# Kernel tuning notes

Measured on AMD Instinct MI355X. Metric: run time of the kernel, lower is better.

## Reference

```python
import jax, jax.numpy as jnp
import numpy as np

N, M, DIST, HEADS, D, C, DFFN = 16384, 16, 2, 8, 256, 64, 512
DH = D // HEADS
GRID = 128
BLOCK = 2048  # mirrors torch batch_size loop in find_neighboring_voxels_optimized
EPS = 1e-5


def _neighbors(coords_f, src, m, dist):
    """Blockwise Manhattan-distance topk neighbor gather.
    coords_f: (N,3) float voxel coords; src: (N,D) features.
    Returns (N, m, D) neighbor features, zero-filled where fewer than m in range."""
    n = coords_f.shape[0]
    qblocks = coords_f.reshape(-1, BLOCK, 3)

    def one_block(cb):
        # (BLOCK, N) Manhattan distances
        d = jnp.abs(cb[:, None, :] - coords_f[None, :, :]).sum(-1)
        d = jnp.where(d <= dist, d, jnp.inf)
        vals, idx = jax.lax.top_k(-d, m)          # nearest m (self first: dist 0)
        valid = (vals > -jnp.inf)[..., None]
        return jnp.where(valid, src[idx], jnp.zeros((), src.dtype))

    return jax.lax.map(one_block, qblocks).reshape(n, m, src.shape[-1])


def _layernorm(x, g, b):
    mu = x.mean(-1, keepdims=True)
    var = ((x - mu) ** 2).mean(-1, keepdims=True)
    return (x - mu) * jax.lax.rsqrt(var + EPS) * g + b


def setup_inputs() -> dict:
    key = jax.random.key(0)
    ks = jax.random.split(key, 32)
    p = lambda i, shape, s: jax.random.normal(ks[i], shape, dtype=jnp.float32) * s
    z = lambda shape: jnp.zeros(shape, dtype=jnp.float32)
    o = lambda shape: jnp.ones(shape, dtype=jnp.float32)
    return {
        "coords": jax.random.randint(ks[0], (N, 3), 0, GRID, dtype=jnp.int32),
        "features": jax.random.normal(ks[1], (N, C), dtype=jnp.float32),
        "pe_w1": p(2, (3, D // 2), 0.5), "pe_b1": z((D // 2,)),
        "pe_w2": p(3, (D // 2, D), 0.08), "pe_b2": z((D,)),
        "proj_w": p(4, (C, D), 0.12), "proj_b": z((D,)),
        "wq": p(5, (D, D), 0.06), "bq": z((D,)),
        "wk": p(6, (D, D), 0.06), "bk": z((D,)),
        "wv": p(7, (D, D), 0.06), "bv": z((D,)),
        "wo": p(8, (D, D), 0.06), "bo": z((D,)),
        "ffn_w1": p(9, (D, DFFN), 0.06), "ffn_b1": z((DFFN,)),
        "ffn_w2": p(10, (DFFN, D), 0.04), "ffn_b2": z((D,)),
        "ln_g": o((D,)), "ln_b": z((D,)),
        "fus_w1": p(11, (D, C), 0.06), "fus_b1": z((C,)),
        "fus_w2": p(12, (2 * C, C), 0.09), "fus_b2": z((C,)),
        "bn_g": o((C,)), "bn_b": z((C,)),
    }


def reference(coords, features, pe_w1, pe_b1, pe_w2, pe_b2, proj_w, proj_b,
              wq, bq, wk, bk, wv, bv, wo, bo,
              ffn_w1, ffn_b1, ffn_w2, ffn_b2, ln_g, ln_b,
              fus_w1, fus_b1, fus_w2, fus_b2, bn_g, bn_b):
    coords_f = coords.astype(jnp.float32)
    # dynamic learnable positional encoding on normalized coords
    xn = coords_f / (GRID - 1)
    pe = jax.nn.relu(xn @ pe_w1 + pe_b1) @ pe_w2 + pe_b2
    src = features @ proj_w + proj_b + pe                       # (N, D)

    nf = _neighbors(coords_f, src, M, DIST)                     # (N, M, D)
    query = nf[:, 0, :]                                         # (N, D) self-feature

    # multihead attention: query len 1, key len M, batch N
    q = (query @ wq + bq).reshape(N, HEADS, DH)
    k = (nf @ wk + bk).reshape(N, M, HEADS, DH)
    v = (nf @ wv + bv).reshape(N, M, HEADS, DH)
    scores = jnp.einsum('nhd,nmhd->nhm', q, k) / jnp.sqrt(jnp.float32(DH))
    attn = jax.nn.softmax(scores, axis=-1)
    ao = jnp.einsum('nhm,nmhd->nhd', attn, v).reshape(N, D) @ wo + bo  # (N, D)

    # FFN with residual + LayerNorm (dropout=0 / eval)
    h = jax.nn.relu(ao @ ffn_w1 + ffn_b1) @ ffn_w2 + ffn_b2
    y = _layernorm(ao + h, ln_g, ln_b)                          # (N, D)

    # EnhancedFusion: project, concat, linear, BatchNorm1d (batch stats), ReLU
    t = y @ fus_w1 + fus_b1                                     # (N, C)
    f = jnp.concatenate([features, t], axis=1) @ fus_w2 + fus_b2
    mu = f.mean(0)
    var = ((f - mu) ** 2).mean(0)
    f = (f - mu) * jax.lax.rsqrt(var + EPS) * bn_g + bn_b
    return jax.nn.relu(f)                                       # (N, C)
```

## Files before the change

kernel.cpp:

```cpp
#include <hip/hip_runtime.h>
#include <stdint.h>

typedef unsigned short u16;
typedef unsigned int   u32;
typedef __attribute__((ext_vector_type(8))) short short8;
typedef __attribute__((ext_vector_type(4))) float f32x4;

static constexpr int kN = 16384;
static constexpr float kEPS = 1e-5f;

__device__ __forceinline__ u16 f2bf(float x) {
  u32 u = __float_as_uint(x);
  u32 r = (u + 0x7fffu + ((u >> 16) & 1u)) >> 16;
  return (u16)r;
}
__device__ __forceinline__ float bf2f(u16 x) {
  return __uint_as_float(((u32)x) << 16);
}
__device__ __forceinline__ void ldbf8(const u16* p, float* o) {
  uint4 v = *(const uint4*)p;
  o[0] = __uint_as_float(v.x << 16);  o[1] = __uint_as_float(v.x & 0xffff0000u);
  o[2] = __uint_as_float(v.y << 16);  o[3] = __uint_as_float(v.y & 0xffff0000u);
  o[4] = __uint_as_float(v.z << 16);  o[5] = __uint_as_float(v.z & 0xffff0000u);
  o[6] = __uint_as_float(v.w << 16);  o[7] = __uint_as_float(v.w & 0xffff0000u);
}


__global__ __launch_bounds__(256) void k_hist(const int* __restrict__ coords,
                                              u32* __restrict__ cnt) {
  int n = blockIdx.x * 256 + threadIdx.x;
  int c = coords[n * 3] * 128 + coords[n * 3 + 1];
  atomicAdd(&cnt[c], 1u);
}

__global__ __launch_bounds__(256) void k_scan(const u32* __restrict__ cnt,
                                              u32* __restrict__ startb) {
  __shared__ u32 tots[256];
  int t = threadIdx.x;
  int base = t * 64;
  u32 s = 0;
  for (int i = 0; i < 64; i++) s += cnt[base + i];
  tots[t] = s;
  __syncthreads();
  if (t == 0) {
    u32 run = 0;
    for (int i = 0; i < 256; i++) { u32 v = tots[i]; tots[i] = run; run += v; }
  }
  __syncthreads();
  u32 run = tots[t];
  for (int i = 0; i < 64; i++) { startb[base + i] = run; run += cnt[base + i]; }
}

__global__ __launch_bounds__(256) void k_scatter(const int* __restrict__ coords,
                                                 const u32* __restrict__ startb,
                                                 u32* __restrict__ cursor,
                                                 u32* __restrict__ pts) {
  int n = blockIdx.x * 256 + threadIdx.x;
  int x = coords[n * 3], y = coords[n * 3 + 1], z = coords[n * 3 + 2];
  int c = x * 128 + y;
  u32 slot = atomicAdd(&cursor[c], 1u);
  pts[startb[c] + slot] = ((u32)z << 14) | (u32)n;
}

__global__ __launch_bounds__(256) void k_select(const int* __restrict__ coords,
                                                const u32* __restrict__ startb,
                                                const u32* __restrict__ cnt,
                                                const u32* __restrict__ pts,
                                                int* __restrict__ idxo) {
  int n = blockIdx.x * 256 + threadIdx.x;
  int x = coords[n * 3], y = coords[n * 3 + 1], z = coords[n * 3 + 2];
  u32 best[16];
#pragma unroll
  for (int j = 0; j < 16; j++) best[j] = 0xFFFFFFFFu;
  const int dxs[13] = {0, -1, 1, 0, 0, -2, 2, 0, 0, -1, -1, 1, 1};
  const int dys[13] = {0, 0, 0, -1, 1, 0, 0, -2, 2, -1, 1, -1, 1};
  const int dbs[13] = {0, 1, 1, 1, 1, 2, 2, 2, 2, 2, 2, 2, 2};
#pragma unroll
  for (int t = 0; t < 13; t++) {
    int xx = x + dxs[t], yy = y + dys[t];
    if (xx < 0 || xx > 127 || yy < 0 || yy > 127) continue;
    int c = xx * 128 + yy;
    u32 s0 = startb[c], e0 = s0 + cnt[c];
    for (u32 i = s0; i < e0; ++i) {
      u32 p = pts[i];
      int zq = (int)(p >> 14);
      int id = (int)(p & 16383u);
      int az = z - zq; az = az < 0 ? -az : az;
      int dd = dbs[t] + az;
      u32 key = (dd <= 2) ? (((u32)dd << 14) | (u32)id) : 0xFFFFFFFFu;
#pragma unroll
      for (int j = 0; j < 16; j++) {
        u32 lo = min(best[j], key);
        u32 hi = max(best[j], key);
        best[j] = lo; key = hi;
      }
    }
  }
#pragma unroll
  for (int j = 0; j < 16; j++)
    idxo[n * 16 + j] = (best[j] == 0xFFFFFFFFu) ? -1 : (int)(best[j] & 16383u);
}

struct WSet {
  const float* s[8]; u16* d[8];
  int K[8]; int N[8]; int dstride[8]; int coff[8];
};

__global__ __launch_bounds__(256) void k_setup(WSet ws,
                                               u32* __restrict__ zero_area,
                                               const float* __restrict__ proj_b,
                                               const float* __restrict__ pe_b2,
                                               float* __restrict__ pbc,
                                               const float* __restrict__ uw1,
                                               const float* __restrict__ ub1,
                                               const float* __restrict__ uw2,
                                               const float* __restrict__ ub2,
                                               u16* __restrict__ W2f,
                                               float* __restrict__ bbf) {
  int w = blockIdx.y;
  if (w == 8) {
    zero_area[blockIdx.x * 256 + threadIdx.x] = 0u;
    return;
  }
  if (w == 9) {
    int bx = blockIdx.x;
    if (bx == 0) {
      pbc[threadIdx.x] = proj_b[threadIdx.x] + pe_b2[threadIdx.x];
    } else if (bx < 65) {
      int n = bx - 1;
      int k = threadIdx.x;
      float s = 0.f;
      for (int j = 0; j < 64; j++) s += uw1[k * 64 + j] * uw2[(64 + j) * 64 + n];
      W2f[n * 320 + k] = f2bf(s);
      if (k < 64) W2f[n * 320 + 256 + k] = f2bf(uw2[k * 64 + n]);
      if (k == 0) {
        float b = ub2[n];
        for (int j = 0; j < 64; j++) b += ub1[j] * uw2[(64 + j) * 64 + n];
        bbf[n] = b;
      }
    }
    return;
  }
  const float* S = ws.s[w]; u16* D = ws.d[w];
  int K = ws.K[w], N = ws.N[w], ds = ws.dstride[w], co = ws.coff[w];
  int ntx = N >> 5, tiles = ntx * (K >> 5);
  int t = blockIdx.x;
  if (t >= tiles) return;
  int n0 = (t % ntx) * 32, k0 = (t / ntx) * 32;
  __shared__ float st[32][33];
  int tr = threadIdx.x >> 3, tc4 = (threadIdx.x & 7) * 4;
  float4 v = *(const float4*)(S + (size_t)(k0 + tr) * N + n0 + tc4);
  st[tc4 + 0][tr] = v.x; st[tc4 + 1][tr] = v.y;
  st[tc4 + 2][tr] = v.z; st[tc4 + 3][tr] = v.w;
  __syncthreads();
  u16 o4[4];
  o4[0] = f2bf(st[tr][tc4 + 0]); o4[1] = f2bf(st[tr][tc4 + 1]);
  o4[2] = f2bf(st[tr][tc4 + 2]); o4[3] = f2bf(st[tr][tc4 + 3]);
  *(uint2*)(D + (size_t)(n0 + tr) * ds + co + k0 + tc4) = *(uint2*)o4;
}

__global__ __launch_bounds__(256) void k_prep(const int* __restrict__ coords,
                                              const float* __restrict__ feats,
                                              const float* __restrict__ pw1,
                                              const float* __restrict__ pb1,
                                              u16* __restrict__ A1,
                                              u16* __restrict__ A2) {
  int r0 = blockIdx.x * 32;
#pragma unroll
  for (int s = 0; s < 3; s++) {
    int j = threadIdx.x + s * 256;
    int row = j / 24, seg = j % 24;
    int n = r0 + row;
    u16 o[8];
    if (seg < 8) {
      const float* fp = feats + (size_t)n * 64 + seg * 8;
      float4 a = *(const float4*)fp;
      float4 b = *(const float4*)(fp + 4);
      o[0] = f2bf(a.x); o[1] = f2bf(a.y); o[2] = f2bf(a.z); o[3] = f2bf(a.w);
      o[4] = f2bf(b.x); o[5] = f2bf(b.y); o[6] = f2bf(b.z); o[7] = f2bf(b.w);
      *(uint4*)(A2 + (size_t)n * 320 + 256 + seg * 8) = *(uint4*)o;
    } else {
      int jj0 = (seg - 8) * 8;
      float x0 = (float)coords[n * 3 + 0] * (1.f / 127.f);
      float x1 = (float)coords[n * 3 + 1] * (1.f / 127.f);
      float x2 = (float)coords[n * 3 + 2] * (1.f / 127.f);
#pragma unroll
      for (int u = 0; u < 8; u++) {
        int jj = jj0 + u;
        float hv = pb1[jj] + x0 * pw1[jj] + x1 * pw1[128 + jj] + x2 * pw1[256 + jj];
        o[u] = f2bf(fmaxf(hv, 0.f));
      }
    }
    *(uint4*)(A1 + (size_t)n * 192 + seg * 8) = *(uint4*)o;
  }
}

template <int BM, int BN, int ACT, int OUTBF, int ADD>
__global__ __launch_bounds__(256) void k_mfma_gemm(
    const u16* __restrict__ A, const u16* __restrict__ WT,
    const float* __restrict__ bias,
    void* __restrict__ Cout,
    const u16* __restrict__ Addp,
    int M, int K, int N) {
  constexpr int GA = BM / 64;
  constexpr int GT = (BM + BN) / 64;
  constexpr int AI = BM / 32;
  constexpr int BI = BN / 32;
  __shared__ __align__(16) u16 As[BM * 32];
  __shared__ __align__(16) u16 Bs[BN * 32];
  const int tid = threadIdx.x;
  const int wave = tid >> 6, lane = tid & 63;
  const int bm = blockIdx.y * BM, bn = blockIdx.x * BN;
  const int wr = (wave >> 1) * (BM / 2), wc = (wave & 1) * (BN / 2);

  f32x4 acc[AI][BI];
#pragma unroll
  for (int i = 0; i < AI; i++)
#pragma unroll
    for (int j = 0; j < BI; j++)
#pragma unroll
      for (int r = 0; r < 4; r++) acc[i][j][r] = 0.f;

  for (int k0 = 0; k0 < K; k0 += 32) {
#pragma unroll
    for (int i = 0; i < GT; i++) {
      int g = i * 256 + wave * 64 + lane;
      if (i < GA) {
        int row = g >> 2, ko = (g & 3) * 8;
        __builtin_amdgcn_global_load_lds(
            (const __attribute__((address_space(1))) void*)(A + (size_t)(bm + row) * K + k0 + ko),
            (__attribute__((address_space(3))) void*)(As + (size_t)g * 8), 16, 0, 0);
      } else {
        int g2 = g - GA * 256;
        int row = g2 >> 2, ko = (g2 & 3) * 8;
        __builtin_amdgcn_global_load_lds(
            (const __attribute__((address_space(1))) void*)(WT + (size_t)(bn + row) * K + k0 + ko),
            (__attribute__((address_space(3))) void*)(Bs + (size_t)g2 * 8), 16, 0, 0);
      }
    }
    __syncthreads();
    short8 af[AI], bg[BI];
#pragma unroll
    for (int i = 0; i < AI; i++)
      af[i] = *(const short8*)&As[(wr + i * 16 + (lane & 15)) * 32 + (lane >> 4) * 8];
#pragma unroll
    for (int j = 0; j < BI; j++)
      bg[j] = *(const short8*)&Bs[(wc + j * 16 + (lane & 15)) * 32 + (lane >> 4) * 8];
#pragma unroll
    for (int i = 0; i < AI; i++)
#pragma unroll
      for (int j = 0; j < BI; j++)
        acc[i][j] = __builtin_amdgcn_mfma_f32_16x16x32_bf16(af[i], bg[j], acc[i][j], 0, 0, 0);
    __syncthreads();
  }

#pragma unroll
  for (int j = 0; j < BI; j++) {
    int cc = bn + wc + j * 16 + (lane & 15);
    float bval = bias ? bias[cc] : 0.f;
#pragma unroll
    for (int i = 0; i < AI; i++) {
      int rbase = bm + wr + i * 16 + (lane >> 4) * 4;
#pragma unroll
      for (int r = 0; r < 4; r++) {
        float v = acc[i][j][r] + bval;
        size_t o = (size_t)(rbase + r) * N + cc;
        if (ADD) v += bf2f(Addp[o]);
        if (ACT) v = fmaxf(v, 0.f);
        if (OUTBF) ((u16*)Cout)[o] = f2bf(v);
        else       ((float*)Cout)[o] = v;
      }
    }
  }
}

__global__ __launch_bounds__(256) void k_attn(const u16* __restrict__ QKV,
                                              const u32* __restrict__ pts,
                                              const int* __restrict__ idx,
                                              const float* __restrict__ bq,
                                              const float* __restrict__ bk,
                                              const float* __restrict__ bv,
                                              u16* __restrict__ outp) {
  int gid = blockIdx.x * 256 + threadIdx.x;
  int n = (int)(pts[gid >> 3] & 16383u), h = gid & 7;
  const int* ip = idx + n * 16;
  const int hb = h * 32;
  float q[32];
  {
    int i0 = ip[0];
    const u16* qp = QKV + (size_t)i0 * 768 + hb;
#pragma unroll
    for (int j = 0; j < 32; j += 8) ldbf8(qp + j, &q[j]);
#pragma unroll
    for (int j = 0; j < 32; j++) q[j] += bq[hb + j];
  }
  float qbk = 0.f;
#pragma unroll
  for (int j = 0; j < 32; j++) qbk += q[j] * bk[hb + j];
  float s[16]; int ii[16];
#pragma unroll
  for (int m = 0; m < 16; m++) {
    int i = ip[m]; ii[m] = i;
    float d = qbk;
    if (i >= 0) {
      const u16* kp = QKV + (size_t)i * 768 + 256 + hb;
      float kv[32];
#pragma unroll
      for (int j = 0; j < 32; j += 8) ldbf8(kp + j, &kv[j]);
#pragma unroll
      for (int j = 0; j < 32; j++) d += q[j] * kv[j];
    }
    s[m] = d * 0.17677669529663689f;
  }
  float mx = s[0];
#pragma unroll
  for (int m = 1; m < 16; m++) mx = fmaxf(mx, s[m]);
  float sum = 0.f;
#pragma unroll
  for (int m = 0; m < 16; m++) { s[m] = __expf(s[m] - mx); sum += s[m]; }
  float inv = 1.f / sum;
  float o[32];
#pragma unroll
  for (int j = 0; j < 32; j++) o[j] = 0.f;
#pragma unroll
  for (int m = 0; m < 16; m++) {
    if (ii[m] >= 0) {
      const u16* vp = QKV + (size_t)ii[m] * 768 + 512 + hb;
      float vv[32];
#pragma unroll
      for (int j = 0; j < 32; j += 8) ldbf8(vp + j, &vv[j]);
#pragma unroll
      for (int j = 0; j < 32; j++) o[j] += s[m] * vv[j];
    }
  }
  u16* op = outp + (size_t)n * 256 + hb;
#pragma unroll
  for (int j = 0; j < 32; j += 8) {
    u16 tmp[8];
#pragma unroll
    for (int jj = 0; jj < 8; jj++) tmp[jj] = f2bf(o[j + jj] * inv + bv[hb + j + jj]);
    *(uint4*)(op + j) = *(uint4*)tmp;
  }
}

__global__ __launch_bounds__(256) void k_ln(const u16* __restrict__ xx,
                                            const float* __restrict__ g,
                                            const float* __restrict__ b,
                                            u16* __restrict__ A2) {
  int row = blockIdx.x * 4 + (threadIdx.x >> 6);
  int lane = threadIdx.x & 63;
  uint2 raw = *(const uint2*)(xx + (size_t)row * 256 + lane * 4);
  float x0 = __uint_as_float(raw.x << 16), x1 = __uint_as_float(raw.x & 0xffff0000u);
  float x2 = __uint_as_float(raw.y << 16), x3 = __uint_as_float(raw.y & 0xffff0000u);
  float sm = x0 + x1 + x2 + x3;
#pragma unroll
  for (int off = 1; off < 64; off <<= 1) sm += __shfl_xor(sm, off);
  float mu = sm * (1.f / 256.f);
  float d0 = x0 - mu, d1 = x1 - mu, d2 = x2 - mu, d3 = x3 - mu;
  float sq = d0 * d0 + d1 * d1 + d2 * d2 + d3 * d3;
#pragma unroll
  for (int off = 1; off < 64; off <<= 1) sq += __shfl_xor(sq, off);
  float rstd = rsqrtf(sq * (1.f / 256.f) + kEPS);
  float4 gv = *(const float4*)(g + lane * 4);
  float4 bv4 = *(const float4*)(b + lane * 4);
  u16 o[4];
  o[0] = f2bf(d0 * rstd * gv.x + bv4.x); o[1] = f2bf(d1 * rstd * gv.y + bv4.y);
  o[2] = f2bf(d2 * rstd * gv.z + bv4.z); o[3] = f2bf(d3 * rstd * gv.w + bv4.w);
  *(uint2*)(A2 + (size_t)row * 320 + lane * 4) = *(uint2*)o;
}

__global__ __launch_bounds__(256) void k_stats(const float* __restrict__ f,
                                               float* __restrict__ pS, float* __restrict__ pQ) {
  int col = threadIdx.x & 63, rc = threadIdx.x >> 6;
  int r0 = blockIdx.x * 128 + rc * 32;
  float s = 0.f, q = 0.f;
  for (int r = 0; r < 32; r++) {
    float v = f[(size_t)(r0 + r) * 64 + col];
    s += v; q += v * v;
  }
  __shared__ float ls[4][64], lq[4][64];
  ls[rc][col] = s; lq[rc][col] = q;
  __syncthreads();
  if (rc == 0) {
    s = ls[0][col] + ls[1][col] + ls[2][col] + ls[3][col];
    q = lq[0][col] + lq[1][col] + lq[2][col] + lq[3][col];
    pS[blockIdx.x * 64 + col] = s;
    pQ[blockIdx.x * 64 + col] = q;
  }
}

__global__ __launch_bounds__(64) void k_bnfin(const float* __restrict__ pS,
                                              const float* __restrict__ pQ,
                                              const float* __restrict__ g,
                                              const float* __restrict__ b,
                                              float* __restrict__ coef,
                                              float* __restrict__ shift) {
  int c = threadIdx.x;
  float s = 0.f, q = 0.f;
  for (int i = 0; i < 128; i++) { s += pS[i * 64 + c]; q += pQ[i * 64 + c]; }
  float mu = s * (1.f / 16384.f);
  float var = q * (1.f / 16384.f) - mu * mu;
  float cf = rsqrtf(var + kEPS) * g[c];
  coef[c] = cf;
  shift[c] = b[c] - mu * cf;
}

__global__ __launch_bounds__(256) void k_bnapply(const float* __restrict__ f,
                                                 const float* __restrict__ coef,
                                                 const float* __restrict__ shift,
                                                 float* __restrict__ out) {
  int gid = blockIdx.x * 256 + threadIdx.x;
  int e = gid * 4, col = e & 63;
  float4 v = *(const float4*)(f + e);
  float4 cf = *(const float4*)(coef + col);
  float4 sh = *(const float4*)(shift + col);
  float4 o;
  o.x = fmaxf(v.x * cf.x + sh.x, 0.f);
  o.y = fmaxf(v.y * cf.y + sh.y, 0.f);
  o.z = fmaxf(v.z * cf.z + sh.z, 0.f);
  o.w = fmaxf(v.w * cf.w + sh.w, 0.f);
  *(float4*)(out + e) = o;
}

extern "C" void kernel_launch(void* const* d_in, const int* in_sizes, int n_in,
                              void* d_out, int out_size, void* d_ws, size_t ws_size,
                              hipStream_t stream) {
  (void)in_sizes; (void)n_in; (void)out_size; (void)ws_size;
  const int*   coords = (const int*)d_in[0];
  const float* feats  = (const float*)d_in[1];
  const float* pe_w1  = (const float*)d_in[2];
  const float* pe_b1  = (const float*)d_in[3];
  const float* pe_w2  = (const float*)d_in[4];
  const float* pe_b2  = (const float*)d_in[5];
  const float* proj_w = (const float*)d_in[6];
  const float* proj_b = (const float*)d_in[7];
  const float* wq  = (const float*)d_in[8];
  const float* bq  = (const float*)d_in[9];
  const float* wk  = (const float*)d_in[10];
  const float* bk  = (const float*)d_in[11];
  const float* wv  = (const float*)d_in[12];
  const float* bv  = (const float*)d_in[13];
  const float* wo  = (const float*)d_in[14];
  const float* bo  = (const float*)d_in[15];
  const float* fw1 = (const float*)d_in[16];
  const float* fb1 = (const float*)d_in[17];
  const float* fw2 = (const float*)d_in[18];
  const float* fb2 = (const float*)d_in[19];
  const float* lng = (const float*)d_in[20];
  const float* lnb = (const float*)d_in[21];
  const float* uw1 = (const float*)d_in[22];
  const float* ub1 = (const float*)d_in[23];
  const float* uw2 = (const float*)d_in[24];
  const float* ub2 = (const float*)d_in[25];
  const float* bng = (const float*)d_in[26];
  const float* bnb = (const float*)d_in[27];
  float* out = (float*)d_out;

  char* Wc = (char*)d_ws;
  const size_t MB = 1u << 20;
  u16*   A1    = (u16*)(Wc + 0 * MB);
  u16*   srcb  = (u16*)(Wc + 6 * MB);
  u16*   QKVb  = (u16*)(Wc + 14 * MB);
  u16*   aoInB = (u16*)(Wc + 38 * MB);
  u16*   aoB   = (u16*)(Wc + 46 * MB);
  u16*   h1B   = (u16*)(Wc + 54 * MB);
  u16*   xBb   = (u16*)(Wc + 70 * MB);
  u16*   A2    = (u16*)(Wc + 78 * MB);
  float* fB    = (float*)(Wc + 0 * MB);

  u16* qkvT  = (u16*)(Wc + 96 * MB);
  u16* woT   = qkvT + 196608;
  u16* fw1T  = woT + 65536;
  u16* fw2T  = fw1T + 131072;
  u16* W1T   = fw2T + 131072;
  u16* W2f   = W1T + 49152;
  float* pbc = (float*)(W2f + 20480);
  float* bbf = pbc + 256;

  u32* cnt    = (u32*)(Wc + 98 * MB);
  u32* cursor = cnt + 16384;
  u32* startb = cnt + 32768;
  u32* pts    = cnt + 49152;
  int* idxb   = (int*)(cnt + 65536);
  float* pS    = (float*)(cnt + 65536 + 262144);
  float* pQ    = pS + 8192;
  float* coefb = pQ + 8192;
  float* shb   = coefb + 64;

  WSet ws;
  ws.s[0] = wq;     ws.d[0] = qkvT;          ws.K[0] = 256; ws.N[0] = 256; ws.dstride[0] = 256; ws.coff[0] = 0;
  ws.s[1] = wk;     ws.d[1] = qkvT + 65536;  ws.K[1] = 256; ws.N[1] = 256; ws.dstride[1] = 256; ws.coff[1] = 0;
  ws.s[2] = wv;     ws.d[2] = qkvT + 131072; ws.K[2] = 256; ws.N[2] = 256; ws.dstride[2] = 256; ws.coff[2] = 0;
  ws.s[3] = wo;     ws.d[3] = woT;           ws.K[3] = 256; ws.N[3] = 256; ws.dstride[3] = 256; ws.coff[3] = 0;
  ws.s[4] = fw1;    ws.d[4] = fw1T;          ws.K[4] = 256; ws.N[4] = 512; ws.dstride[4] = 256; ws.coff[4] = 0;
  ws.s[5] = fw2;    ws.d[5] = fw2T;          ws.K[5] = 512; ws.N[5] = 256; ws.dstride[5] = 512; ws.coff[5] = 0;
  ws.s[6] = proj_w; ws.d[6] = W1T;           ws.K[6] = 64;  ws.N[6] = 256; ws.dstride[6] = 192; ws.coff[6] = 0;
  ws.s[7] = pe_w2;  ws.d[7] = W1T;           ws.K[7] = 128; ws.N[7] = 256; ws.dstride[7] = 192; ws.coff[7] = 64;
  k_setup<<<dim3(128, 10), 256, 0, stream>>>(ws, cnt, proj_b, pe_b2, pbc,
                                             uw1, ub1, uw2, ub2, W2f, bbf);

  k_hist<<<64, 256, 0, stream>>>(coords, cnt);
  k_scan<<<1, 256, 0, stream>>>(cnt, startb);
  k_scatter<<<64, 256, 0, stream>>>(coords, startb, cursor, pts);
  k_select<<<64, 256, 0, stream>>>(coords, startb, cnt, pts, idxb);

  k_prep<<<512, 256, 0, stream>>>(coords, feats, pe_w1, pe_b1, A1, A2);

  k_mfma_gemm<64, 64, 0, 1, 0><<<dim3(4, 256), 256, 0, stream>>>(A1, W1T, pbc, srcb, nullptr, kN, 192, 256);
  k_mfma_gemm<64, 64, 0, 1, 0><<<dim3(12, 256), 256, 0, stream>>>(srcb, qkvT, nullptr, QKVb, nullptr, kN, 256, 768);

  k_attn<<<512, 256, 0, stream>>>(QKVb, pts, idxb, bq, bk, bv, aoInB);

  k_mfma_gemm<64, 64, 0, 1, 0><<<dim3(4, 256), 256, 0, stream>>>(aoInB, woT, bo, aoB, nullptr, kN, 256, 256);
  k_mfma_gemm<64, 64, 1, 1, 0><<<dim3(8, 256), 256, 0, stream>>>(aoB, fw1T, fb1, h1B, nullptr, kN, 256, 512);
  k_mfma_gemm<64, 64, 0, 1, 1><<<dim3(4, 256), 256, 0, stream>>>(h1B, fw2T, fb2, xBb, aoB, kN, 512, 256);

  k_ln<<<4096, 256, 0, stream>>>(xBb, lng, lnb, A2);

  k_mfma_gemm<64, 64, 0, 0, 0><<<dim3(1, 256), 256, 0, stream>>>(A2, W2f, bbf, fB, nullptr, kN, 320, 64);

  k_stats<<<128, 256, 0, stream>>>(fB, pS, pQ);
  k_bnfin<<<1, 64, 0, stream>>>(pS, pQ, bng, bnb, coefb, shb);
  k_bnapply<<<1024, 256, 0, stream>>>(fB, coefb, shb, out);
}
```

Before: 257.6 us.

## Fuse neighbor-grid stages and BN tail into persistent kernels with grid barriers

Merges the histogram, scan, scatter and select kernels into one 64-block kernel that uses software grid barriers built on atomics. The final GEMM, batch-norm statistics, finalize and apply steps become one kernel that keeps its results in registers and uses a last-arriving block to compute the BN coefficients. The prep kernel is folded into the setup launch. This cuts kernel launch count and drops the fp32 intermediate round trip. In exchange it depends on all blocks being co-resident for the spin-wait barriers, and the float atomicAdd reductions make the statistics order nondeterministic.

After: 294.6 us. 1.14x slower.

```diff
diff --git a/kernel.cpp b/kernel.cpp
--- a/kernel.cpp
+++ b/kernel.cpp
@@ -24,81 +24,10 @@
   o[4] = __uint_as_float(v.z << 16);  o[5] = __uint_as_float(v.z & 0xffff0000u);
   o[6] = __uint_as_float(v.w << 16);  o[7] = __uint_as_float(v.w & 0xffff0000u);
 }
-
-
-__global__ __launch_bounds__(256) void k_hist(const int* __restrict__ coords,
-                                              u32* __restrict__ cnt) {
-  int n = blockIdx.x * 256 + threadIdx.x;
-  int c = coords[n * 3] * 128 + coords[n * 3 + 1];
-  atomicAdd(&cnt[c], 1u);
-}
-
-__global__ __launch_bounds__(256) void k_scan(const u32* __restrict__ cnt,
-                                              u32* __restrict__ startb) {
-  __shared__ u32 tots[256];
-  int t = threadIdx.x;
-  int base = t * 64;
-  u32 s = 0;
-  for (int i = 0; i < 64; i++) s += cnt[base + i];
-  tots[t] = s;
-  __syncthreads();
-  if (t == 0) {
-    u32 run = 0;
-    for (int i = 0; i < 256; i++) { u32 v = tots[i]; tots[i] = run; run += v; }
-  }
-  __syncthreads();
-  u32 run = tots[t];
-  for (int i = 0; i < 64; i++) { startb[base + i] = run; run += cnt[base + i]; }
-}
-
-__global__ __launch_bounds__(256) void k_scatter(const int* __restrict__ coords,
-                                                 const u32* __restrict__ startb,
-                                                 u32* __restrict__ cursor,
-                                                 u32* __restrict__ pts) {
-  int n = blockIdx.x * 256 + threadIdx.x;
-  int x = coords[n * 3], y = coords[n * 3 + 1], z = coords[n * 3 + 2];
-  int c = x * 128 + y;
-  u32 slot = atomicAdd(&cursor[c], 1u);
-  pts[startb[c] + slot] = ((u32)z << 14) | (u32)n;
-}
-
-__global__ __launch_bounds__(256) void k_select(const int* __restrict__ coords,
-                                                const u32* __restrict__ startb,
-                                                const u32* __restrict__ cnt,
-                                                const u32* __restrict__ pts,
-                                                int* __restrict__ idxo) {
-  int n = blockIdx.x * 256 + threadIdx.x;
-  int x = coords[n * 3], y = coords[n * 3 + 1], z = coords[n * 3 + 2];
-  u32 best[16];
-#pragma unroll
-  for (int j = 0; j < 16; j++) best[j] = 0xFFFFFFFFu;
-  const int dxs[13] = {0, -1, 1, 0, 0, -2, 2, 0, 0, -1, -1, 1, 1};
-  const int dys[13] = {0, 0, 0, -1, 1, 0, 0, -2, 2, -1, 1, -1, 1};
-  const int dbs[13] = {0, 1, 1, 1, 1, 2, 2, 2, 2, 2, 2, 2, 2};
-#pragma unroll
-  for (int t = 0; t < 13; t++) {
-    int xx = x + dxs[t], yy = y + dys[t];
-    if (xx < 0 || xx > 127 || yy < 0 || yy > 127) continue;
-    int c = xx * 128 + yy;
-    u32 s0 = startb[c], e0 = s0 + cnt[c];
-    for (u32 i = s0; i < e0; ++i) {
-      u32 p = pts[i];
-      int zq = (int)(p >> 14);
-      int id = (int)(p & 16383u);
-      int az = z - zq; az = az < 0 ? -az : az;
-      int dd = dbs[t] + az;
-      u32 key = (dd <= 2) ? (((u32)dd << 14) | (u32)id) : 0xFFFFFFFFu;
-#pragma unroll
-      for (int j = 0; j < 16; j++) {
-        u32 lo = min(best[j], key);
-        u32 hi = max(best[j], key);
-        best[j] = lo; key = hi;
-      }
-    }
-  }
-#pragma unroll
-  for (int j = 0; j < 16; j++)
-    idxo[n * 16 + j] = (best[j] == 0xFFFFFFFFu) ? -1 : (int)(best[j] & 16383u);
+__device__ __forceinline__ void gll16(const u16* g, u16* l) {
+  __builtin_amdgcn_global_load_lds(
+      (const __attribute__((address_space(1))) void*)g,
+      (__attribute__((address_space(3))) void*)l, 16, 0, 0);
 }
 
 struct WSet {
@@ -116,10 +45,17 @@
                                                const float* __restrict__ uw2,
                                                const float* __restrict__ ub2,
                                                u16* __restrict__ W2f,
-                                               float* __restrict__ bbf) {
+                                               float* __restrict__ bbf,
+                                               const int* __restrict__ coords,
+                                               const float* __restrict__ feats,
+                                               const float* __restrict__ pw1,
+                                               const float* __restrict__ pb1,
+                                               u16* __restrict__ A1,
+                                               u16* __restrict__ A2) {
   int w = blockIdx.y;
   if (w == 8) {
-    zero_area[blockIdx.x * 256 + threadIdx.x] = 0u;
+    int idx = blockIdx.x * 256 + threadIdx.x;
+    if (idx < 33088) zero_area[idx] = 0u;
     return;
   }
   if (w == 9) {
@@ -141,6 +77,37 @@
     }
     return;
   }
+  if (w == 10) {
+    int r0 = blockIdx.x * 32;
+#pragma unroll
+    for (int s = 0; s < 3; s++) {
+      int j = threadIdx.x + s * 256;
+      int row = j / 24, seg = j % 24;
+      int n = r0 + row;
+      u16 o[8];
+      if (seg < 8) {
+        const float* fp = feats + (size_t)n * 64 + seg * 8;
+        float4 a = *(const float4*)fp;
+        float4 b = *(const float4*)(fp + 4);
+        o[0] = f2bf(a.x); o[1] = f2bf(a.y); o[2] = f2bf(a.z); o[3] = f2bf(a.w);
+        o[4] = f2bf(b.x); o[5] = f2bf(b.y); o[6] = f2bf(b.z); o[7] = f2bf(b.w);
+        *(uint4*)(A2 + (size_t)n * 320 + 256 + seg * 8) = *(uint4*)o;
+      } else {
+        int jj0 = (seg - 8) * 8;
+        float x0 = (float)coords[n * 3 + 0] * (1.f / 127.f);
+        float x1 = (float)coords[n * 3 + 1] * (1.f / 127.f);
+        float x2 = (float)coords[n * 3 + 2] * (1.f / 127.f);
+#pragma unroll
+        for (int u = 0; u < 8; u++) {
+          int jj = jj0 + u;
+          float hv = pb1[jj] + x0 * pw1[jj] + x1 * pw1[128 + jj] + x2 * pw1[256 + jj];
+          o[u] = f2bf(fmaxf(hv, 0.f));
+        }
+      }
+      *(uint4*)(A1 + (size_t)n * 192 + seg * 8) = *(uint4*)o;
+    }
+    return;
+  }
   const float* S = ws.s[w]; u16* D = ws.d[w];
   int K = ws.K[w], N = ws.N[w], ds = ws.dstride[w], co = ws.coff[w];
   int ntx = N >> 5, tiles = ntx * (K >> 5);
@@ -159,108 +126,136 @@
   *(uint2*)(D + (size_t)(n0 + tr) * ds + co + k0 + tc4) = *(uint2*)o4;
 }
 
-__global__ __launch_bounds__(256) void k_prep(const int* __restrict__ coords,
-                                              const float* __restrict__ feats,
-                                              const float* __restrict__ pw1,
-                                              const float* __restrict__ pb1,
-                                              u16* __restrict__ A1,
-                                              u16* __restrict__ A2) {
-  int r0 = blockIdx.x * 32;
-#pragma unroll
-  for (int s = 0; s < 3; s++) {
-    int j = threadIdx.x + s * 256;
-    int row = j / 24, seg = j % 24;
-    int n = r0 + row;
-    u16 o[8];
-    if (seg < 8) {
-      const float* fp = feats + (size_t)n * 64 + seg * 8;
-      float4 a = *(const float4*)fp;
-      float4 b = *(const float4*)(fp + 4);
-      o[0] = f2bf(a.x); o[1] = f2bf(a.y); o[2] = f2bf(a.z); o[3] = f2bf(a.w);
-      o[4] = f2bf(b.x); o[5] = f2bf(b.y); o[6] = f2bf(b.z); o[7] = f2bf(b.w);
-      *(uint4*)(A2 + (size_t)n * 320 + 256 + seg * 8) = *(uint4*)o;
-    } else {
-      int jj0 = (seg - 8) * 8;
-      float x0 = (float)coords[n * 3 + 0] * (1.f / 127.f);
-      float x1 = (float)coords[n * 3 + 1] * (1.f / 127.f);
-      float x2 = (float)coords[n * 3 + 2] * (1.f / 127.f);
-#pragma unroll
-      for (int u = 0; u < 8; u++) {
-        int jj = jj0 + u;
-        float hv = pb1[jj] + x0 * pw1[jj] + x1 * pw1[128 + jj] + x2 * pw1[256 + jj];
-        o[u] = f2bf(fmaxf(hv, 0.f));
+__device__ __forceinline__ void gbar(u32* bar, u32 target) {
+  __syncthreads();
+  if (threadIdx.x == 0) {
+    __threadfence();
+    __hip_atomic_fetch_add(bar, 1u, __ATOMIC_RELEASE, __HIP_MEMORY_SCOPE_AGENT);
+    while (__hip_atomic_load(bar, __ATOMIC_ACQUIRE, __HIP_MEMORY_SCOPE_AGENT) < target) {}
+    __threadfence();
+  }
+  __syncthreads();
+}
+
+__global__ __launch_bounds__(256) void k_grid(const int* __restrict__ coords,
+                                              u32* __restrict__ cnt,
+                                              u32* __restrict__ cursor,
+                                              u32* __restrict__ startb,
+                                              u32* __restrict__ pts,
+                                              int* __restrict__ idxo,
+                                              u32* __restrict__ bar) {
+  int n = blockIdx.x * 256 + threadIdx.x;
+  int x = coords[n * 3], y = coords[n * 3 + 1], z = coords[n * 3 + 2];
+  int c = x * 128 + y;
+  atomicAdd(&cnt[c], 1u);
+  gbar(bar, 64);
+  if (blockIdx.x == 0) {
+    __shared__ u32 tots[256];
+    int t = threadIdx.x;
+    int base = t * 64;
+    u32 s = 0;
+    for (int i = 0; i < 64; i++) s += cnt[base + i];
+    tots[t] = s;
+    __syncthreads();
+    if (t == 0) {
+      u32 run = 0;
+      for (int i = 0; i < 256; i++) { u32 v = tots[i]; tots[i] = run; run += v; }
+    }
+    __syncthreads();
+    u32 run = tots[t];
+    for (int i = 0; i < 64; i++) { startb[base + i] = run; run += cnt[base + i]; }
+  }
+  gbar(bar, 128);
+  {
+    u32 slot = atomicAdd(&cursor[c], 1u);
+    pts[startb[c] + slot] = ((u32)z << 14) | (u32)n;
+  }
+  gbar(bar, 192);
+  {
+    u32 best[16];
+#pragma unroll
+    for (int j = 0; j < 16; j++) best[j] = 0xFFFFFFFFu;
+    const int dxs[13] = {0, -1, 1, 0, 0, -2, 2, 0, 0, -1, -1, 1, 1};
+    const int dys[13] = {0, 0, 0, -1, 1, 0, 0, -2, 2, -1, 1, -1, 1};
+    const int dbs[13] = {0, 1, 1, 1, 1, 2, 2, 2, 2, 2, 2, 2, 2};
+#pragma unroll
+    for (int t = 0; t < 13; t++) {
+      int xx = x + dxs[t], yy = y + dys[t];
+      if (xx < 0 || xx > 127 || yy < 0 || yy > 127) continue;
+      int cc = xx * 128 + yy;
+      u32 s0 = startb[cc], e0 = s0 + cnt[cc];
+      for (u32 i = s0; i < e0; ++i) {
+        u32 p = pts[i];
+        int zq = (int)(p >> 14);
+        int id = (int)(p & 16383u);
+        int az = z - zq; az = az < 0 ? -az : az;
+        int dd = dbs[t] + az;
+        u32 key = (dd <= 2) ? (((u32)dd << 14) | (u32)id) : 0xFFFFFFFFu;
+#pragma unroll
+        for (int j = 0; j < 16; j++) {
+          u32 lo = min(best[j], key);
+          u32 hi = max(best[j], key);
+          best[j] = lo; key = hi;
+        }
       }
     }
-    *(uint4*)(A1 + (size_t)n * 192 + seg * 8) = *(uint4*)o;
-  }
-}
-
-template <int BM, int BN, int ACT, int OUTBF, int ADD>
+#pragma unroll
+    for (int j = 0; j < 16; j++)
+      idxo[n * 16 + j] = (best[j] == 0xFFFFFFFFu) ? -1 : (int)(best[j] & 16383u);
+  }
+}
+
+template <int ACT, int OUTBF, int ADD>
 __global__ __launch_bounds__(256) void k_mfma_gemm(
     const u16* __restrict__ A, const u16* __restrict__ WT,
     const float* __restrict__ bias,
     void* __restrict__ Cout,
     const u16* __restrict__ Addp,
     int M, int K, int N) {
-  constexpr int GA = BM / 64;
-  constexpr int GT = (BM + BN) / 64;
-  constexpr int AI = BM / 32;
-  constexpr int BI = BN / 32;
-  __shared__ __align__(16) u16 As[BM * 32];
-  __shared__ __align__(16) u16 Bs[BN * 32];
+  __shared__ __align__(16) u16 As[64 * 32];
+  __shared__ __align__(16) u16 Bs[64 * 32];
   const int tid = threadIdx.x;
   const int wave = tid >> 6, lane = tid & 63;
-  const int bm = blockIdx.y * BM, bn = blockIdx.x * BN;
-  const int wr = (wave >> 1) * (BM / 2), wc = (wave & 1) * (BN / 2);
-
-  f32x4 acc[AI][BI];
-#pragma unroll
-  for (int i = 0; i < AI; i++)
-#pragma unroll
-    for (int j = 0; j < BI; j++)
+  const int bm = blockIdx.y * 64, bn = blockIdx.x * 64;
+  const int wr = (wave >> 1) * 32, wc = (wave & 1) * 32;
+  const int g = wave * 64 + lane;
+  const int grow = g >> 2, gko = (g & 3) * 8;
+  const int fr = lane & 15, fk = (lane >> 4) * 8, rq = (lane >> 4) * 4;
+
+  f32x4 acc[2][2];
+#pragma unroll
+  for (int i = 0; i < 2; i++)
+#pragma unroll
+    for (int j = 0; j < 2; j++)
 #pragma unroll
       for (int r = 0; r < 4; r++) acc[i][j][r] = 0.f;
 
   for (int k0 = 0; k0 < K; k0 += 32) {
-#pragma unroll
-    for (int i = 0; i < GT; i++) {
-      int g = i * 256 + wave * 64 + lane;
-      if (i < GA) {
-        int row = g >> 2, ko = (g & 3) * 8;
-        __builtin_amdgcn_global_load_lds(
-            (const __attribute__((address_space(1))) void*)(A + (size_t)(bm + row) * K + k0 + ko),
-            (__attribute__((address_space(3))) void*)(As + (size_t)g * 8), 16, 0, 0);
-      } else {
-        int g2 = g - GA * 256;
-        int row = g2 >> 2, ko = (g2 & 3) * 8;
-        __builtin_amdgcn_global_load_lds(
-            (const __attribute__((address_space(1))) void*)(WT + (size_t)(bn + row) * K + k0 + ko),
-            (__attribute__((address_space(3))) void*)(Bs + (size_t)g2 * 8), 16, 0, 0);
-      }
-    }
-    __syncthreads();
-    short8 af[AI], bg[BI];
-#pragma unroll
-    for (int i = 0; i < AI; i++)
-      af[i] = *(const short8*)&As[(wr + i * 16 + (lane & 15)) * 32 + (lane >> 4) * 8];
-#pragma unroll
-    for (int j = 0; j < BI; j++)
-      bg[j] = *(const short8*)&Bs[(wc + j * 16 + (lane & 15)) * 32 + (lane >> 4) * 8];
-#pragma unroll
-    for (int i = 0; i < AI; i++)
-#pragma unroll
-      for (int j = 0; j < BI; j++)
+    gll16(A + (size_t)(bm + grow) * K + k0 + gko, As + g * 8);
+    gll16(WT + (size_t)(bn + grow) * K + k0 + gko, Bs + g * 8);
+    __syncthreads();
+    short8 af[2], bg[2];
+#pragma unroll
+    for (int i = 0; i < 2; i++)
+      af[i] = *(const short8*)&As[(wr + i * 16 + fr) * 32 + fk];
+#pragma unroll
+    for (int j = 0; j < 2; j++)
+      bg[j] = *(const short8*)&Bs[(wc + j * 16 + fr) * 32 + fk];
+#pragma unroll
+    for (int i = 0; i < 2; i++)
+#pragma unroll
+      for (int j = 0; j < 2; j++)
         acc[i][j] = __builtin_amdgcn_mfma_f32_16x16x32_bf16(af[i], bg[j], acc[i][j], 0, 0, 0);
     __syncthreads();
   }
 
 #pragma unroll
-  for (int j = 0; j < BI; j++) {
-    int cc = bn + wc + j * 16 + (lane & 15);
+  for (int j = 0; j < 2; j++) {
+    int cc = bn + wc + j * 16 + fr;
     float bval = bias ? bias[cc] : 0.f;
 #pragma unroll
-    for (int i = 0; i < AI; i++) {
-      int rbase = bm + wr + i * 16 + (lane >> 4) * 4;
+    for (int i = 0; i < 2; i++) {
+      int rbase = bm + wr + i * 16 + rq;
 #pragma unroll
       for (int r = 0; r < 4; r++) {
         float v = acc[i][j][r] + bval;
@@ -369,57 +364,130 @@
   *(uint2*)(A2 + (size_t)row * 320 + lane * 4) = *(uint2*)o;
 }
 
-__global__ __launch_bounds__(256) void k_stats(const float* __restrict__ f,
-                                               float* __restrict__ pS, float* __restrict__ pQ) {
-  int col = threadIdx.x & 63, rc = threadIdx.x >> 6;
-  int r0 = blockIdx.x * 128 + rc * 32;
-  float s = 0.f, q = 0.f;
-  for (int r = 0; r < 32; r++) {
-    float v = f[(size_t)(r0 + r) * 64 + col];
-    s += v; q += v * v;
-  }
-  __shared__ float ls[4][64], lq[4][64];
-  ls[rc][col] = s; lq[rc][col] = q;
-  __syncthreads();
-  if (rc == 0) {
-    s = ls[0][col] + ls[1][col] + ls[2][col] + ls[3][col];
-    q = lq[0][col] + lq[1][col] + lq[2][col] + lq[3][col];
-    pS[blockIdx.x * 64 + col] = s;
-    pQ[blockIdx.x * 64 + col] = q;
-  }
-}
-
-__global__ __launch_bounds__(64) void k_bnfin(const float* __restrict__ pS,
-                                              const float* __restrict__ pQ,
-                                              const float* __restrict__ g,
-                                              const float* __restrict__ b,
+__global__ __launch_bounds__(256) void k_tail(const u16* __restrict__ A2,
+                                              const u16* __restrict__ W2f,
+                                              const float* __restrict__ bbf,
+                                              float* __restrict__ pS,
+                                              float* __restrict__ pQ,
+                                              u32* __restrict__ arrive,
+                                              u32* __restrict__ done,
+                                              const float* __restrict__ bng,
+                                              const float* __restrict__ bnb,
                                               float* __restrict__ coef,
-                                              float* __restrict__ shift) {
-  int c = threadIdx.x;
-  float s = 0.f, q = 0.f;
-  for (int i = 0; i < 128; i++) { s += pS[i * 64 + c]; q += pQ[i * 64 + c]; }
-  float mu = s * (1.f / 16384.f);
-  float var = q * (1.f / 16384.f) - mu * mu;
-  float cf = rsqrtf(var + kEPS) * g[c];
-  coef[c] = cf;
-  shift[c] = b[c] - mu * cf;
-}
-
-__global__ __launch_bounds__(256) void k_bnapply(const float* __restrict__ f,
-                                                 const float* __restrict__ coef,
-                                                 const float* __restrict__ shift,
-                                                 float* __restrict__ out) {
-  int gid = blockIdx.x * 256 + threadIdx.x;
-  int e = gid * 4, col = e & 63;
-  float4 v = *(const float4*)(f + e);
-  float4 cf = *(const float4*)(coef + col);
-  float4 sh = *(const float4*)(shift + col);
-  float4 o;
-  o.x = fmaxf(v.x * cf.x + sh.x, 0.f);
-  o.y = fmaxf(v.y * cf.y + sh.y, 0.f);
-  o.z = fmaxf(v.z * cf.z + sh.z, 0.f);
-  o.w = fmaxf(v.w * cf.w + sh.w, 0.f);
-  *(float4*)(out + e) = o;
+                                              float* __restrict__ shift,
+                                              float* __restrict__ out) {
+  __shared__ __align__(16) u16 As[2048];
+  __shared__ __align__(16) u16 Bs[2048];
+  __shared__ float colS[64][2], colQ[64][2];
+  __shared__ u32 lastf;
+  const int tid = threadIdx.x;
+  const int wave = tid >> 6, lane = tid & 63;
+  const int bm = blockIdx.x * 64;
+  const int wr = (wave >> 1) * 32, wc = (wave & 1) * 32;
+  const int fr = lane & 15, fk = (lane >> 4) * 8, rq = (lane >> 4) * 4;
+  const int g = wave * 64 + lane;
+  const int grow = g >> 2, gko = (g & 3) * 8;
+
+  f32x4 acc[2][2];
+#pragma unroll
+  for (int i = 0; i < 2; i++)
+#pragma unroll
+    for (int j = 0; j < 2; j++)
+#pragma unroll
+      for (int r = 0; r < 4; r++) acc[i][j][r] = 0.f;
+  for (int k0 = 0; k0 < 320; k0 += 32) {
+    gll16(A2 + (size_t)(bm + grow) * 320 + k0 + gko, As + g * 8);
+    gll16(W2f + (size_t)grow * 320 + k0 + gko, Bs + g * 8);
+    __syncthreads();
+    short8 af[2], bg[2];
+#pragma unroll
+    for (int i = 0; i < 2; i++)
+      af[i] = *(const short8*)&As[(wr + i * 16 + fr) * 32 + fk];
+#pragma unroll
+    for (int j = 0; j < 2; j++)
+      bg[j] = *(const short8*)&Bs[(wc + j * 16 + fr) * 32 + fk];
+#pragma unroll
+    for (int i = 0; i < 2; i++)
+#pragma unroll
+      for (int j = 0; j < 2; j++)
+        acc[i][j] = __builtin_amdgcn_mfma_f32_16x16x32_bf16(af[i], bg[j], acc[i][j], 0, 0, 0);
+    __syncthreads();
+  }
+  float cS[2] = {0.f, 0.f}, cQ[2] = {0.f, 0.f};
+#pragma unroll
+  for (int j = 0; j < 2; j++) {
+    int col = wc + j * 16 + fr;
+    float bv = bbf[col];
+#pragma unroll
+    for (int i = 0; i < 2; i++)
+#pragma unroll
+      for (int r = 0; r < 4; r++) {
+        float v = acc[i][j][r] + bv;
+        acc[i][j][r] = v;
+        cS[j] += v; cQ[j] += v * v;
+      }
+  }
+#pragma unroll
+  for (int off = 16; off < 64; off <<= 1) {
+#pragma unroll
+    for (int j = 0; j < 2; j++) {
+      cS[j] += __shfl_xor(cS[j], off);
+      cQ[j] += __shfl_xor(cQ[j], off);
+    }
+  }
+  if ((lane >> 4) == 0) {
+#pragma unroll
+    for (int j = 0; j < 2; j++) {
+      colS[wc + j * 16 + fr][wave >> 1] = cS[j];
+      colQ[wc + j * 16 + fr][wave >> 1] = cQ[j];
+    }
+  }
+  __syncthreads();
+  if (tid < 64) {
+    atomicAdd(&pS[tid], colS[tid][0] + colS[tid][1]);
+    atomicAdd(&pQ[tid], colQ[tid][0] + colQ[tid][1]);
+  }
+  __syncthreads();
+  if (tid == 0) {
+    __threadfence();
+    u32 old = __hip_atomic_fetch_add(arrive, 1u, __ATOMIC_ACQ_REL, __HIP_MEMORY_SCOPE_AGENT);
+    lastf = (old == 255) ? 1u : 0u;
+  }
+  __syncthreads();
+  if (lastf) {
+    if (tid < 64) {
+      float S = __hip_atomic_load(&pS[tid], __ATOMIC_ACQUIRE, __HIP_MEMORY_SCOPE_AGENT);
+      float Q = __hip_atomic_load(&pQ[tid], __ATOMIC_ACQUIRE, __HIP_MEMORY_SCOPE_AGENT);
+      float m = S * (1.f / 16384.f);
+      float var = Q * (1.f / 16384.f) - m * m;
+      float cf = rsqrtf(var + kEPS) * bng[tid];
+      __hip_atomic_store(&coef[tid], cf, __ATOMIC_RELAXED, __HIP_MEMORY_SCOPE_AGENT);
+      __hip_atomic_store(&shift[tid], bnb[tid] - m * cf, __ATOMIC_RELAXED, __HIP_MEMORY_SCOPE_AGENT);
+    }
+    __syncthreads();
+    if (tid == 0) {
+      __threadfence();
+      __hip_atomic_store(done, 1u, __ATOMIC_RELEASE, __HIP_MEMORY_SCOPE_AGENT);
+    }
+  }
+  if (tid == 0) {
+    while (__hip_atomic_load(done, __ATOMIC_ACQUIRE, __HIP_MEMORY_SCOPE_AGENT) == 0u) {}
+    __threadfence();
+  }
+  __syncthreads();
+#pragma unroll
+  for (int j = 0; j < 2; j++) {
+    int col = wc + j * 16 + fr;
+    float cf = __hip_atomic_load(&coef[col], __ATOMIC_RELAXED, __HIP_MEMORY_SCOPE_AGENT);
+    float sh = __hip_atomic_load(&shift[col], __ATOMIC_RELAXED, __HIP_MEMORY_SCOPE_AGENT);
+#pragma unroll
+    for (int i = 0; i < 2; i++) {
+      int rbase = bm + wr + i * 16 + rq;
+#pragma unroll
+      for (int r = 0; r < 4; r++)
+        out[(size_t)(rbase + r) * 64 + col] = fmaxf(acc[i][j][r] * cf + sh, 0.f);
+    }
+  }
 }
 
 extern "C" void kernel_launch(void* const* d_in, const int* in_sizes, int n_in,
@@ -466,9 +534,8 @@
   u16*   h1B   = (u16*)(Wc + 54 * MB);
   u16*   xBb   = (u16*)(Wc + 70 * MB);
   u16*   A2    = (u16*)(Wc + 78 * MB);
-  float* fB    = (float*)(Wc + 0 * MB);
-
-  u16* qkvT  = (u16*)(Wc + 96 * MB);
+
+  u16* qkvT  = (u16*)(Wc + 88 * MB);
   u16* woT   = qkvT + 196608;
   u16* fw1T  = woT + 65536;
   u16* fw2T  = fw1T + 131072;
@@ -477,15 +544,19 @@
   float* pbc = (float*)(W2f + 20480);
   float* bbf = pbc + 256;
 
-  u32* cnt    = (u32*)(Wc + 98 * MB);
-  u32* cursor = cnt + 16384;
-  u32* startb = cnt + 32768;
-  u32* pts    = cnt + 49152;
-  int* idxb   = (int*)(cnt + 65536);
-  float* pS    = (float*)(cnt + 65536 + 262144);
-  float* pQ    = pS + 8192;
-  float* coefb = pQ + 8192;
+  u32* Z      = (u32*)(Wc + 90 * MB);
+  u32* cnt    = Z;
+  u32* cursor = Z + 16384;
+  float* pS   = (float*)(Z + 32768);
+  float* pQ   = (float*)(Z + 32832);
+  u32* bar    = Z + 32896;
+  u32* arrive = Z + 32897;
+  u32* done   = Z + 32898;
+  float* coefb = (float*)(Z + 32912);
   float* shb   = coefb + 64;
+  u32* startb = Z + 33280;
+  u32* pts    = Z + 49664;
+  int* idxb   = (int*)(Z + 66048);
 
   WSet ws;
   ws.s[0] = wq;     ws.d[0] = qkvT;          ws.K[0] = 256; ws.N[0] = 256; ws.dstride[0] = 256; ws.coff[0] = 0;
@@ -496,30 +567,17 @@
   ws.s[5] = fw2;    ws.d[5] = fw2T;          ws.K[5] = 512; ws.N[5] = 256; ws.dstride[5] = 512; ws.coff[5] = 0;
   ws.s[6] = proj_w; ws.d[6] = W1T;           ws.K[6] = 64;  ws.N[6] = 256; ws.dstride[6] = 192; ws.coff[6] = 0;
   ws.s[7] = pe_w2;  ws.d[7] = W1T;           ws.K[7] = 128; ws.N[7] = 256; ws.dstride[7] = 192; ws.coff[7] = 64;
-  k_setup<<<dim3(128, 10), 256, 0, stream>>>(ws, cnt, proj_b, pe_b2, pbc,
-                                             uw1, ub1, uw2, ub2, W2f, bbf);
-
-  k_hist<<<64, 256, 0, stream>>>(coords, cnt);
-  k_scan<<<1, 256, 0, stream>>>(cnt, startb);
-  k_scatter<<<64, 256, 0, stream>>>(coords, startb, cursor, pts);
-  k_select<<<64, 256, 0, stream>>>(coords, startb, cnt, pts, idxb);
-
-  k_prep<<<512, 256, 0, stream>>>(coords, feats, pe_w1, pe_b1, A1, A2);
-
-  k_mfma_gemm<64, 64, 0, 1, 0><<<dim3(4, 256), 256, 0, stream>>>(A1, W1T, pbc, srcb, nullptr, kN, 192, 256);
-  k_mfma_gemm<64, 64, 0, 1, 0><<<dim3(12, 256), 256, 0, stream>>>(srcb, qkvT, nullptr, QKVb, nullptr, kN, 256, 768);
-
+
+  k_setup<<<dim3(512, 11), 256, 0, stream>>>(ws, Z, proj_b, pe_b2, pbc,
+                                             uw1, ub1, uw2, ub2, W2f, bbf,
+                                             coords, feats, pe_w1, pe_b1, A1, A2);
+  k_grid<<<64, 256, 0, stream>>>(coords, cnt, cursor, startb, pts, idxb, bar);
+  k_mfma_gemm<0, 1, 0><<<dim3(4, 256), 256, 0, stream>>>(A1, W1T, pbc, srcb, nullptr, kN, 192, 256);
+  k_mfma_gemm<0, 1, 0><<<dim3(12, 256), 256, 0, stream>>>(srcb, qkvT, nullptr, QKVb, nullptr, kN, 256, 768);
   k_attn<<<512, 256, 0, stream>>>(QKVb, pts, idxb, bq, bk, bv, aoInB);
-
-  k_mfma_gemm<64, 64, 0, 1, 0><<<dim3(4, 256), 256, 0, stream>>>(aoInB, woT, bo, aoB, nullptr, kN, 256, 256);
-  k_mfma_gemm<64, 64, 1, 1, 0><<<dim3(8, 256), 256, 0, stream>>>(aoB, fw1T, fb1, h1B, nullptr, kN, 256, 512);
-  k_mfma_gemm<64, 64, 0, 1, 1><<<dim3(4, 256), 256, 0, stream>>>(h1B, fw2T, fb2, xBb, aoB, kN, 512, 256);
-
+  k_mfma_gemm<0, 1, 0><<<dim3(4, 256), 256, 0, stream>>>(aoInB, woT, bo, aoB, nullptr, kN, 256, 256);
+  k_mfma_gemm<1, 1, 0><<<dim3(8, 256), 256, 0, stream>>>(aoB, fw1T, fb1, h1B, nullptr, kN, 256, 512);
+  k_mfma_gemm<0, 1, 1><<<dim3(4, 256), 256, 0, stream>>>(h1B, fw2T, fb2, xBb, aoB, kN, 512, 256);
   k_ln<<<4096, 256, 0, stream>>>(xBb, lng, lnb, A2);
-
-  k_mfma_gemm<64, 64, 0, 0, 0><<<dim3(1, 256), 256, 0, stream>>>(A2, W2f, bbf, fB, nullptr, kN, 320, 64);
-
-  k_stats<<<128, 256, 0, stream>>>(fB, pS, pQ);
-  k_bnfin<<<1, 64, 0, stream>>>(pS, pQ, bng, bnb, coefb, shb);
-  k_bnapply<<<1024, 256, 0, stream>>>(fB, coefb, shb, out);
-}
+  k_tail<<<256, 256, 0, stream>>>(A2, W2f, bbf, pS, pQ, arrive, done, bng, bnb, coefb, shb, out);
+}
```
